# Kernel tuning notes

Hardware: AMD Instinct MI355X
Metric: run time of the kernel (lower is better)

The kernel has to match this reference:

```python
import jax, jax.numpy as jnp
import numpy as np

K = 3       # kernel size
PAD = 1     # k // 2
S = 1       # stride
EPS = 1e-5  # BatchNorm eps


def setup_inputs() -> dict:
    key = jax.random.key(0)
    ks = jax.random.split(key, 7)
    B, C1, C2, H, W = 4, 256, 256, 80, 80
    x = jax.random.normal(ks[0], (B, C1, H, W), dtype=jnp.float32)
    # offset/mask conv params (orig inits these to zero; use small random so
    # the deformable sampling path is actually exercised)
    w_off = jax.random.normal(ks[1], (3 * K * K, C1, K, K), dtype=jnp.float32) * 0.01
    b_off = jax.random.normal(ks[2], (3 * K * K,), dtype=jnp.float32) * 0.01
    weight = jax.random.normal(ks[3], (C2, C1, K, K), dtype=jnp.float32) * 0.05
    bias = jax.random.normal(ks[4], (C2,), dtype=jnp.float32) * 0.05
    gamma = jnp.ones((C2,), dtype=jnp.float32)
    beta = jnp.zeros((C2,), dtype=jnp.float32)
    return {"x": x, "w_off": w_off, "b_off": b_off, "weight": weight,
            "bias": bias, "gamma": gamma, "beta": beta}


def _elastic_head(x, w_off, b_off, weight, bias, gamma, beta):
    B, C, H, W = x.shape
    K2 = K * K
    # offset/mask predictor conv (stride 1, SAME padding -> output H x W)
    off_out = jax.lax.conv_general_dilated(
        x, w_off, (S, S), 'SAME',
        dimension_numbers=('NCHW', 'OIHW', 'NCHW')) + b_off[None, :, None, None]
    o1, o2, m = off_out[:, :K2], off_out[:, K2:2 * K2], off_out[:, 2 * K2:]
    mask = jax.nn.sigmoid(m)                                   # [B,K2,H,W]
    # torchvision layout: channel 2p = dy_p, 2p+1 = dx_p
    off = jnp.concatenate([o1, o2], axis=1).reshape(B, K2, 2, H, W)
    dy, dx = off[:, :, 0], off[:, :, 1]                        # [B,K2,H,W]
    # base sampling grid per kernel tap
    ii, jj = jnp.meshgrid(jnp.arange(K), jnp.arange(K), indexing='ij')
    ii = ii.reshape(K2)
    jj = jj.reshape(K2)
    base_y = (jnp.arange(H)[None, :] * S - PAD + ii[:, None]).astype(x.dtype)  # [K2,H]
    base_x = (jnp.arange(W)[None, :] * S - PAD + jj[:, None]).astype(x.dtype)  # [K2,W]
    ys = dy + base_y[None, :, :, None]                         # [B,K2,H,W]
    xs = dx + base_x[None, :, None, :]
    y0 = jnp.floor(ys)
    x0 = jnp.floor(xs)
    wy = ys - y0
    wx = xs - x0
    y0i = y0.astype(jnp.int32)
    x0i = x0.astype(jnp.int32)
    y1i = y0i + 1
    x1i = x0i + 1
    x_flat = x.reshape(B, C, H * W)

    def gather(yy, xx):
        valid = ((yy >= 0) & (yy < H) & (xx >= 0) & (xx < W)).astype(x.dtype)
        idx = jnp.clip(yy, 0, H - 1) * W + jnp.clip(xx, 0, W - 1)
        g = jax.vmap(lambda xf, ix: xf[:, ix])(x_flat, idx.reshape(B, -1))
        return g.reshape(B, C, K2, H, W) * valid[:, None]

    # bilinear sample with zero padding outside, accumulate corners
    patches = (gather(y0i, x0i) * ((1 - wy) * (1 - wx))[:, None]
               + gather(y0i, x1i) * ((1 - wy) * wx)[:, None]
               + gather(y1i, x0i) * (wy * (1 - wx))[:, None]
               + gather(y1i, x1i) * (wy * wx)[:, None])       # [B,C,K2,H,W]
    patches = patches * mask[:, None]                          # modulation
    # implicit GEMM of deform_conv2d
    out = jnp.einsum('bcphw,ocp->bohw', patches,
                     weight.reshape(weight.shape[0], C, K2)) + bias[None, :, None, None]
    # BatchNorm2d (training-mode batch stats, biased variance) + SiLU
    mean = out.mean(axis=(0, 2, 3))
    var = out.var(axis=(0, 2, 3))
    xn = (out - mean[None, :, None, None]) * jax.lax.rsqrt(var + EPS)[None, :, None, None]
    y_bn = xn * gamma[None, :, None, None] + beta[None, :, None, None]
    return y_bn * jax.nn.sigmoid(y_bn)


def reference(x, w_off, b_off, weight, bias, gamma, beta):
    return _elastic_head(x, w_off, b_off, weight, bias, gamma, beta)
```

## Files before the change

### kernel.cpp

```cpp
#include <hip/hip_runtime.h>
#include <math.h>

constexpr int Hc = 80, Wc = 80, Bn = 4, C1 = 256, C2 = 256;
constexpr int HWn = Hc * Wc;
constexpr int NPIX = Bn * HWn;
constexpr int OFFC = 27;
constexpr int KK   = 2304;

typedef short bf16x8 __attribute__((ext_vector_type(8)));
typedef float f32x4  __attribute__((ext_vector_type(4)));

__device__ __forceinline__ unsigned f2bf(float f) {
    unsigned u = __float_as_uint(f);
    return (u + 0x7FFF + ((u >> 16) & 1)) >> 16;
}

__device__ __forceinline__ unsigned packhi2(float v0, float v1) {
    unsigned h;
    asm("v_cvt_pk_bf16_f32 %0, %1, %2" : "=v"(h) : "v"(v0), "v"(v1));
    return h;
}

__device__ __forceinline__ void ub4(uint2 u, float f[4]) {
    f[0] = __uint_as_float(u.x << 16);
    f[1] = __uint_as_float(u.x & 0xffff0000u);
    f[2] = __uint_as_float(u.y << 16);
    f[3] = __uint_as_float(u.y & 0xffff0000u);
}

__global__ __launch_bounds__(256) void k_wprep2(const float* __restrict__ weight,
                                                const float* __restrict__ w_off,
                                                unsigned short* __restrict__ wB1,
                                                unsigned short* __restrict__ wOB)
{
    if (blockIdx.x < 2304) {
        int e = blockIdx.x * 256 + threadIdx.x;
        int kin = e & 7;
        int oc  = (e >> 3) & 255;
        int kg  = (e >> 11) & 3;
        int s   = e >> 13;
        int p   = s >> 3, cc = s & 7;
        float w = weight[((size_t)oc * C1 + cc * 32 + kg * 8 + kin) * 9 + p];
        wB1[e] = (unsigned short)f2bf(w);
    } else {
        int e = (blockIdx.x - 2304) * 256 + threadIdx.x;
        int k  = e & 31;
        int oc = (e >> 5) & 31;
        int s  = e >> 10;
        int p  = s >> 3, cc = s & 7;
        float v = 0.f;
        if (oc < 27) v = w_off[((size_t)oc * C1 + cc * 32 + k) * 9 + p];
        wOB[e] = (unsigned short)f2bf(v);
    }
}

__global__ __launch_bounds__(256) void k_xtrans(const float* __restrict__ x,
                                                unsigned short* __restrict__ xTb)
{
    __shared__ float tile[32][33];
    int bid = blockIdx.x;
    int ct  = bid & 7;
    int hwt = (bid >> 3) % 200;
    int b   = bid / 1600;
    int c0  = ct * 32, hw0 = hwt * 32;
    int tid = threadIdx.x;
    int col = tid & 31, rw = tid >> 5;
    const float* xb = x + (size_t)b * C1 * HWn;
    #pragma unroll
    for (int k = 0; k < 4; ++k) {
        int r = rw + k * 8;
        tile[r][col] = xb[(size_t)(c0 + r) * HWn + hw0 + col];
    }
    __syncthreads();
    unsigned short* xob = xTb + ((size_t)b * HWn + hw0) * C1 + c0;
    #pragma unroll
    for (int k = 0; k < 4; ++k) {
        int r = rw + k * 8;
        xob[(size_t)r * C1 + col] = (unsigned short)f2bf(tile[col][r]);
    }
}

__global__ __launch_bounds__(256) void k_offmeta(const unsigned short* __restrict__ xTb,
                                                 const unsigned short* __restrict__ wOB,
                                                 const float* __restrict__ b_off,
                                                 int* __restrict__ crdbuf,
                                                 float4* __restrict__ w4buf)
{
    __shared__ float offs[32][28];

    int t  = threadIdx.x;
    int wv = t >> 6, lane = t & 63;
    int li = lane & 15, kg = lane >> 4;
    int mi = wv & 1;
    int nj = wv >> 1;

    int mtile = ((blockIdx.x & 7) * 100) + (blockIdx.x >> 3);
    int m0  = mtile * 32;
    int b   = m0 / HWn;
    int hw0 = m0 - b * HWn;
    int pxl = hw0 + mi * 16 + li;
    int h = pxl / Wc, w = pxl - h * Wc;

    const unsigned short* xb = xTb + (size_t)b * HWn * C1;

    f32x4 acc = (f32x4){0.f, 0.f, 0.f, 0.f};
    #pragma unroll
    for (int p = 0; p < 9; ++p) {
        int dh = p / 3 - 1, dw = p % 3 - 1;
        int hh = h + dh, ww = w + dw;
        bool valid = (hh >= 0 && hh < Hc && ww >= 0 && ww < Wc);
        int hwp = valid ? (hh * Wc + ww) : 0;
        const unsigned short* arow = xb + (size_t)hwp * C1 + kg * 8;
        const unsigned short* brow = wOB + ((size_t)(p * 8) * 32 + nj * 16 + li) * 32 + kg * 8;
        #pragma unroll
        for (int cc = 0; cc < 8; ++cc) {
            uint4 av = *(const uint4*)(arow + cc * 32);
            if (!valid) av = make_uint4(0, 0, 0, 0);
            uint4 bv = *(const uint4*)(brow + cc * 1024);
            acc = __builtin_amdgcn_mfma_f32_16x16x32_bf16(
                __builtin_bit_cast(bf16x8, av), __builtin_bit_cast(bf16x8, bv), acc, 0, 0, 0);
        }
    }
    int oc = nj * 16 + li;
    if (oc < OFFC) {
        float bs = b_off[oc];
        #pragma unroll
        for (int r = 0; r < 4; ++r)
            offs[mi * 16 + kg * 4 + r][oc] = acc[r] + bs;
    }
    __syncthreads();

    for (int idx = t; idx < 288; idx += 256) {
        int pix = idx / 9, p = idx - pix * 9;
        int hw  = hw0 + pix;
        int hh = hw / Wc, wwp = hw - hh * Wc;
        int ii = p / 3, jj = p - ii * 3;
        float dy = offs[pix][2 * p];
        float dx = offs[pix][2 * p + 1];
        float mv = offs[pix][18 + p];
        float mask = 1.0f / (1.0f + expf(-mv));
        float ys  = dy + (float)(hh - 1 + ii);
        float xsv = dx + (float)(wwp - 1 + jj);
        float y0f = floorf(ys), x0f = floorf(xsv);
        float wy = ys - y0f, wx = xsv - x0f;
        int y0 = (int)y0f, x0 = (int)x0f;
        int y1 = y0 + 1, x1 = x0 + 1;
        float vy0 = (y0 >= 0 && y0 < Hc) ? 1.f : 0.f;
        float vy1 = (y1 >= 0 && y1 < Hc) ? 1.f : 0.f;
        float vx0 = (x0 >= 0 && x0 < Wc) ? 1.f : 0.f;
        float vx1 = (x1 >= 0 && x1 < Wc) ? 1.f : 0.f;
        float4 wv4;
        wv4.x = mask * (1.f - wy) * (1.f - wx) * vy0 * vx0;
        wv4.y = mask * (1.f - wy) * wx         * vy0 * vx1;
        wv4.z = mask * wy         * (1.f - wx) * vy1 * vx0;
        wv4.w = mask * wy         * wx         * vy1 * vx1;
        int cy0 = min(max(y0, 0), Hc - 1), cy1 = min(max(y1, 0), Hc - 1);
        int cx0 = min(max(x0, 0), Wc - 1), cx1 = min(max(x1, 0), Wc - 1);
        int pair = (m0 + pix) * 9 + p;
        crdbuf[pair] = cy0 | (cy1 << 8) | (cx0 << 16) | (cx1 << 24);
        w4buf[pair]  = wv4;
    }
}

__global__ __launch_bounds__(256) void k_gather(const unsigned short* __restrict__ xTb,
                                                const int* __restrict__ crdbuf,
                                                const float4* __restrict__ w4buf,
                                                unsigned short* __restrict__ Ahi)
{
    int t   = threadIdx.x;
    int wv  = t >> 6, l = t & 63;
    int xcd = blockIdx.x & 7;
    int blk = blockIdx.x >> 3;
    int wgl = (xcd * 400 + blk) * 4 + wv;
    int base = wgl * 18;

    #pragma unroll 2
    for (int i = 0; i < 18; ++i) {
        int pair = base + i;
        int px = pair / 9, p = pair - px * 9;
        int b  = px / HWn;
        int crd = crdbuf[pair];
        float4 w4 = w4buf[pair];
        int cy0 = crd & 255, cy1 = (crd >> 8) & 255;
        int cx0 = (crd >> 16) & 255, cx1 = (crd >> 24) & 255;
        const unsigned short* xt = xTb + (size_t)b * HWn * C1;
        uint2 u00 = ((const uint2*)&xt[(size_t)(cy0 * Wc + cx0) * C1])[l];
        uint2 u01 = ((const uint2*)&xt[(size_t)(cy0 * Wc + cx1) * C1])[l];
        uint2 u10 = ((const uint2*)&xt[(size_t)(cy1 * Wc + cx0) * C1])[l];
        uint2 u11 = ((const uint2*)&xt[(size_t)(cy1 * Wc + cx1) * C1])[l];
        float f00[4], f01[4], f10[4], f11[4];
        ub4(u00, f00); ub4(u01, f01); ub4(u10, f10); ub4(u11, f11);
        float v0 = fmaf(w4.x, f00[0], fmaf(w4.y, f01[0], fmaf(w4.z, f10[0], w4.w * f11[0])));
        float v1 = fmaf(w4.x, f00[1], fmaf(w4.y, f01[1], fmaf(w4.z, f10[1], w4.w * f11[1])));
        float v2 = fmaf(w4.x, f00[2], fmaf(w4.y, f01[2], fmaf(w4.z, f10[2], w4.w * f11[2])));
        float v3 = fmaf(w4.x, f00[3], fmaf(w4.y, f01[3], fmaf(w4.z, f10[3], w4.w * f11[3])));
        unsigned h0 = packhi2(v0, v1), h1 = packhi2(v2, v3);
        int s = p * 8 + (l >> 3);
        size_t aidx = ((size_t)s * NPIX + px) * 32 + 4 * (l & 7);
        *(uint2*)&Ahi[aidx] = make_uint2(h0, h1);
    }
}

__global__ __launch_bounds__(256) void k_dmfma(const unsigned short* __restrict__ Ahi,
                                               const unsigned short* __restrict__ wB1,
                                               const float* __restrict__ bias,
                                               float* __restrict__ out)
{
    __shared__ float Tb[32 * 33];

    int t  = threadIdx.x;
    int wv = t >> 6, lane = t & 63;
    int li = lane & 15, kg = lane >> 4;
    int nh = wv;

    int mtile = ((blockIdx.x & 7) * 100) + (blockIdx.x >> 3);
    int m0  = mtile * 32;
    int b   = m0 / HWn;
    int hw0 = m0 - b * HWn;
    int row0 = m0 + li;
    int row1 = m0 + 16 + li;

    const unsigned short* a0p = Ahi + (size_t)row0 * 32 + kg * 8;
    const unsigned short* a1p = Ahi + (size_t)row1 * 32 + kg * 8;
    const unsigned short* bp  = wB1 + (size_t)(kg * 256 + nh * 64 + li) * 8;

    auto loadA = [&](int s, uint4& h0, uint4& h1) {
        size_t o = (size_t)s * NPIX * 32;
        h0 = *(const uint4*)(a0p + o);
        h1 = *(const uint4*)(a1p + o);
    };
    auto loadB = [&](int s, uint4& b0, uint4& b1, uint4& b2, uint4& b3) {
        const unsigned short* q = bp + (size_t)s * 8192;
        b0 = *(const uint4*)(q);
        b1 = *(const uint4*)(q + 128);
        b2 = *(const uint4*)(q + 256);
        b3 = *(const uint4*)(q + 384);
    };

    f32x4 acc[2][4];
    #pragma unroll
    for (int m = 0; m < 2; ++m)
        #pragma unroll
        for (int n = 0; n < 4; ++n) acc[m][n] = (f32x4){0.f, 0.f, 0.f, 0.f};

    uint4 aA0, aA1, bA0, bA1, bA2, bA3;
    uint4 aB0, aB1, bB0, bB1, bB2, bB3;

    auto compute = [&](uint4& c0, uint4& c1, uint4& q0, uint4& q1, uint4& q2, uint4& q3) {
        bf16x8 a0 = __builtin_bit_cast(bf16x8, c0);
        bf16x8 a1 = __builtin_bit_cast(bf16x8, c1);
        __builtin_amdgcn_s_setprio(1);
        bf16x8 v;
        v = __builtin_bit_cast(bf16x8, q0);
        acc[0][0] = __builtin_amdgcn_mfma_f32_16x16x32_bf16(a0, v, acc[0][0], 0, 0, 0);
        acc[1][0] = __builtin_amdgcn_mfma_f32_16x16x32_bf16(a1, v, acc[1][0], 0, 0, 0);
        v = __builtin_bit_cast(bf16x8, q1);
        acc[0][1] = __builtin_amdgcn_mfma_f32_16x16x32_bf16(a0, v, acc[0][1], 0, 0, 0);
        acc[1][1] = __builtin_amdgcn_mfma_f32_16x16x32_bf16(a1, v, acc[1][1], 0, 0, 0);
        v = __builtin_bit_cast(bf16x8, q2);
        acc[0][2] = __builtin_amdgcn_mfma_f32_16x16x32_bf16(a0, v, acc[0][2], 0, 0, 0);
        acc[1][2] = __builtin_amdgcn_mfma_f32_16x16x32_bf16(a1, v, acc[1][2], 0, 0, 0);
        v = __builtin_bit_cast(bf16x8, q3);
        acc[0][3] = __builtin_amdgcn_mfma_f32_16x16x32_bf16(a0, v, acc[0][3], 0, 0, 0);
        acc[1][3] = __builtin_amdgcn_mfma_f32_16x16x32_bf16(a1, v, acc[1][3], 0, 0, 0);
        __builtin_amdgcn_s_setprio(0);
    };

    loadA(0, aA0, aA1); loadB(0, bA0, bA1, bA2, bA3);
    for (int s = 0; s < 72; s += 2) {
        loadA(s + 1, aB0, aB1); loadB(s + 1, bB0, bB1, bB2, bB3);
        compute(aA0, aA1, bA0, bA1, bA2, bA3);
        if (s + 2 < 72) { loadA(s + 2, aA0, aA1); loadB(s + 2, bA0, bA1, bA2, bA3); }
        compute(aB0, aB1, bB0, bB1, bB2, bB3);
    }

    #pragma unroll
    for (int q = 0; q < 8; ++q) {
        __syncthreads();
        if (nh == (q >> 1)) {
            #pragma unroll
            for (int jj = 0; jj < 2; ++jj) {
                int nt = (q & 1) * 2 + jj;
                #pragma unroll
                for (int m = 0; m < 2; ++m) {
                    f32x4 a = acc[m][nt];
                    int rrw = jj * 16 + li;
                    int col = m * 16 + kg * 4;
                    #pragma unroll
                    for (int r = 0; r < 4; ++r)
                        Tb[rrw * 33 + col + r] = a[r];
                }
            }
        }
        __syncthreads();
        int px = t & 31;
        int rw = t >> 5;
        #pragma unroll
        for (int it = 0; it < 4; ++it) {
            int r  = it * 8 + rw;
            int oc = q * 32 + r;
            out[(size_t)(b * C2 + oc) * HWn + hw0 + px] = Tb[r * 33 + px] + bias[oc];
        }
    }
}

__global__ __launch_bounds__(256) void k_bnpart(const float* __restrict__ out,
                                                float* __restrict__ psum)
{
    int oc = blockIdx.x >> 2;
    int bq = blockIdx.x & 3;
    const float4* src = (const float4*)(out + ((size_t)(bq * C2 + oc)) * HWn);
    float s = 0.f, ss = 0.f;
    for (int i = threadIdx.x; i < 1600; i += 256) {
        float4 v = src[i];
        s  += v.x + v.y + v.z + v.w;
        ss += v.x * v.x + v.y * v.y + v.z * v.z + v.w * v.w;
    }
    __shared__ float ls[256], lss[256];
    ls[threadIdx.x] = s; lss[threadIdx.x] = ss;
    __syncthreads();
    for (int st = 128; st > 0; st >>= 1) {
        if (threadIdx.x < st) {
            ls[threadIdx.x]  += ls[threadIdx.x + st];
            lss[threadIdx.x] += lss[threadIdx.x + st];
        }
        __syncthreads();
    }
    if (threadIdx.x == 0) {
        psum[bq * 256 + oc]        = ls[0];
        psum[1024 + bq * 256 + oc] = lss[0];
    }
}

__global__ __launch_bounds__(256) void k_bnfin(const float* __restrict__ psum,
                                               float* __restrict__ stats)
{
    int oc = threadIdx.x;
    float s  = psum[oc] + psum[256 + oc] + psum[512 + oc] + psum[768 + oc];
    float ss = psum[1024 + oc] + psum[1280 + oc] + psum[1536 + oc] + psum[1792 + oc];
    float mean = s / (float)NPIX;
    float var  = ss / (float)NPIX - mean * mean;
    stats[oc]       = mean;
    stats[256 + oc] = rsqrtf(var + 1e-5f);
}

__global__ __launch_bounds__(256) void k_bnsilu(float* __restrict__ out,
                                                const float* __restrict__ stats,
                                                const float* __restrict__ gamma,
                                                const float* __restrict__ beta)
{
    int n4 = (Bn * C2 * HWn) / 4;
    for (int i = blockIdx.x * blockDim.x + threadIdx.x; i < n4;
         i += gridDim.x * blockDim.x) {
        float4 v = ((float4*)out)[i];
        int e  = i * 4;
        int oc = (e / HWn) & 255;
        float mean = stats[oc];
        float gs   = gamma[oc] * stats[256 + oc];
        float bt   = beta[oc];
        float y;
        y = (v.x - mean) * gs + bt; v.x = y / (1.f + expf(-y));
        y = (v.y - mean) * gs + bt; v.y = y / (1.f + expf(-y));
        y = (v.z - mean) * gs + bt; v.z = y / (1.f + expf(-y));
        y = (v.w - mean) * gs + bt; v.w = y / (1.f + expf(-y));
        ((float4*)out)[i] = v;
    }
}

extern "C" void kernel_launch(void* const* d_in, const int* in_sizes, int n_in,
                              void* d_out, int out_size, void* d_ws, size_t ws_size,
                              hipStream_t stream)
{
    const float* x      = (const float*)d_in[0];
    const float* w_off  = (const float*)d_in[1];
    const float* b_off  = (const float*)d_in[2];
    const float* weight = (const float*)d_in[3];
    const float* bias   = (const float*)d_in[4];
    const float* gamma  = (const float*)d_in[5];
    const float* beta   = (const float*)d_in[6];
    float* out = (float*)d_out;

    char* wsb = (char*)d_ws;
    unsigned short* Ahi  = (unsigned short*)(wsb);
    unsigned short* xTb  = (unsigned short*)(wsb + 117964800);
    unsigned short* wB1  = (unsigned short*)(wsb + 131072000);
    unsigned short* wOB  = (unsigned short*)(wsb + 132251648);
    int*            crdb = (int*)(wsb + 132399104);
    float4*         w4b  = (float4*)(wsb + 133320704);
    float*         stats = (float*)(wsb + 137007104);
    float*         psum  = (float*)(wsb + 137009152);

    k_wprep2  <<<2592, 256, 0, stream>>>(weight, w_off, wB1, wOB);
    k_xtrans  <<<6400, 256, 0, stream>>>(x, xTb);
    k_offmeta <<<800, 256, 0, stream>>>(xTb, wOB, b_off, crdb, w4b);
    k_gather  <<<3200, 256, 0, stream>>>(xTb, crdb, w4b, Ahi);
    k_dmfma   <<<800, 256, 0, stream>>>(Ahi, wB1, bias, out);
    k_bnpart  <<<1024, 256, 0, stream>>>(out, psum);
    k_bnfin   <<<1, 256, 0, stream>>>(psum, stats);
    k_bnsilu  <<<2048, 256, 0, stream>>>(out, stats, gamma, beta);
}
```

Before: 202.5 us.

## Fuse BatchNorm statistics into GEMM epilogue with atomics, drop stats kernels

The GEMM epilogue now reduces per-channel sum and sum-of-squares across each 32-pixel row with wave shuffles and atomically accumulates them into a zeroed buffer. The separate partial-reduction and finalize kernels are removed, and the BN+SiLU kernel computes mean and inverse std into shared memory per block. This avoids re-reading the full 26 MB output and saves two launches. In exchange it adds many float atomics on only 512 addresses, which may contend, and every BN block recomputes the statistics.

Result: slower. 407.9 us (+101.4%).

```diff
diff --git a/kernel.cpp b/kernel.cpp
--- a/kernel.cpp
+++ b/kernel.cpp
@@ -204,7 +204,8 @@
 __global__ __launch_bounds__(256) void k_dmfma(const unsigned short* __restrict__ Ahi,
                                                const unsigned short* __restrict__ wB1,
                                                const float* __restrict__ bias,
-                                               float* __restrict__ out)
+                                               float* __restrict__ out,
+                                               float* __restrict__ psum)
 {
     __shared__ float Tb[32 * 33];
 
@@ -299,64 +300,43 @@
         for (int it = 0; it < 4; ++it) {
             int r  = it * 8 + rw;
             int oc = q * 32 + r;
-            out[(size_t)(b * C2 + oc) * HWn + hw0 + px] = Tb[r * 33 + px] + bias[oc];
+            float v = Tb[r * 33 + px] + bias[oc];
+            out[(size_t)(b * C2 + oc) * HWn + hw0 + px] = v;
+            float s2 = v, ss = v * v;
+            #pragma unroll
+            for (int mk = 16; mk; mk >>= 1) {
+                s2 += __shfl_xor(s2, mk, 32);
+                ss += __shfl_xor(ss, mk, 32);
+            }
+            if (px == 0) {
+                atomicAdd(&psum[oc], s2);
+                atomicAdd(&psum[256 + oc], ss);
+            }
         }
     }
 }
 
-__global__ __launch_bounds__(256) void k_bnpart(const float* __restrict__ out,
-                                                float* __restrict__ psum)
-{
-    int oc = blockIdx.x >> 2;
-    int bq = blockIdx.x & 3;
-    const float4* src = (const float4*)(out + ((size_t)(bq * C2 + oc)) * HWn);
-    float s = 0.f, ss = 0.f;
-    for (int i = threadIdx.x; i < 1600; i += 256) {
-        float4 v = src[i];
-        s  += v.x + v.y + v.z + v.w;
-        ss += v.x * v.x + v.y * v.y + v.z * v.z + v.w * v.w;
-    }
-    __shared__ float ls[256], lss[256];
-    ls[threadIdx.x] = s; lss[threadIdx.x] = ss;
-    __syncthreads();
-    for (int st = 128; st > 0; st >>= 1) {
-        if (threadIdx.x < st) {
-            ls[threadIdx.x]  += ls[threadIdx.x + st];
-            lss[threadIdx.x] += lss[threadIdx.x + st];
-        }
-        __syncthreads();
-    }
-    if (threadIdx.x == 0) {
-        psum[bq * 256 + oc]        = ls[0];
-        psum[1024 + bq * 256 + oc] = lss[0];
-    }
-}
-
-__global__ __launch_bounds__(256) void k_bnfin(const float* __restrict__ psum,
-                                               float* __restrict__ stats)
-{
-    int oc = threadIdx.x;
-    float s  = psum[oc] + psum[256 + oc] + psum[512 + oc] + psum[768 + oc];
-    float ss = psum[1024 + oc] + psum[1280 + oc] + psum[1536 + oc] + psum[1792 + oc];
-    float mean = s / (float)NPIX;
-    float var  = ss / (float)NPIX - mean * mean;
-    stats[oc]       = mean;
-    stats[256 + oc] = rsqrtf(var + 1e-5f);
-}
-
 __global__ __launch_bounds__(256) void k_bnsilu(float* __restrict__ out,
-                                                const float* __restrict__ stats,
+                                                const float* __restrict__ psum,
                                                 const float* __restrict__ gamma,
                                                 const float* __restrict__ beta)
 {
+    __shared__ float sm[256], sv[256];
+    if (threadIdx.x < 256) {
+        float mean = psum[threadIdx.x] / (float)NPIX;
+        float var  = psum[256 + threadIdx.x] / (float)NPIX - mean * mean;
+        sm[threadIdx.x] = mean;
+        sv[threadIdx.x] = rsqrtf(var + 1e-5f);
+    }
+    __syncthreads();
     int n4 = (Bn * C2 * HWn) / 4;
     for (int i = blockIdx.x * blockDim.x + threadIdx.x; i < n4;
          i += gridDim.x * blockDim.x) {
         float4 v = ((float4*)out)[i];
         int e  = i * 4;
         int oc = (e / HWn) & 255;
-        float mean = stats[oc];
-        float gs   = gamma[oc] * stats[256 + oc];
+        float mean = sm[oc];
+        float gs   = gamma[oc] * sv[oc];
         float bt   = beta[oc];
         float y;
         y = (v.x - mean) * gs + bt; v.x = y / (1.f + expf(-y));
@@ -387,15 +367,13 @@
     unsigned short* wOB  = (unsigned short*)(wsb + 132251648);
     int*            crdb = (int*)(wsb + 132399104);
     float4*         w4b  = (float4*)(wsb + 133320704);
-    float*         stats = (float*)(wsb + 137007104);
-    float*         psum  = (float*)(wsb + 137009152);
-
+    float*          psum = (float*)(wsb + 137007104);
+
+    hipMemsetAsync(psum, 0, 2048, stream);
     k_wprep2  <<<2592, 256, 0, stream>>>(weight, w_off, wB1, wOB);
     k_xtrans  <<<6400, 256, 0, stream>>>(x, xTb);
     k_offmeta <<<800, 256, 0, stream>>>(xTb, wOB, b_off, crdb, w4b);
     k_gather  <<<3200, 256, 0, stream>>>(xTb, crdb, w4b, Ahi);
-    k_dmfma   <<<800, 256, 0, stream>>>(Ahi, wB1, bias, out);
-    k_bnpart  <<<1024, 256, 0, stream>>>(out, psum);
-    k_bnfin   <<<1, 256, 0, stream>>>(psum, stats);
-    k_bnsilu  <<<2048, 256, 0, stream>>>(out, stats, gamma, beta);
-}
+    k_dmfma   <<<800, 256, 0, stream>>>(Ahi, wB1, bias, out, psum);
+    k_bnsilu  <<<2048, 256, 0, stream>>>(out, psum, gamma, beta);
+}
```
